# Performance work log

Hardware: AMD Instinct MI355X
Metric: run time of the kernel (lower is better)

The kernel has to match this reference:

```python
import jax, jax.numpy as jnp
import numpy as np

B, H, S, D = 4, 8, 2048, 64
NEG = -1e9


def setup_inputs() -> dict:
    key = jax.random.key(0)
    k1, k2, k3, k4 = jax.random.split(key, 4)
    qs = jax.random.normal(k1, (B, H, S, D), dtype=jnp.float32)
    ks = jax.random.normal(k2, (B, H, S, D), dtype=jnp.float32)
    vs = jax.random.normal(k3, (B, H, S, D), dtype=jnp.float32)
    # binary 0/1 float mask, broadcast over heads
    mask = (jax.random.uniform(k4, (B, 1, S, S)) < 0.5).astype(jnp.float32)
    return {"qs": qs, "ks": ks, "vs": vs, "mask": mask}


def reference(qs, ks, vs, mask):
    scale = 1.0 / np.sqrt(qs.shape[-1]).astype(np.float32)
    # [B,H,S,S] logits; multiplicative pre-mask, then additive -1e9 on masked slots
    logits = jnp.einsum('bhqd,bhkd->bhqk', qs, ks) * mask * scale
    logits = logits + (1.0 - mask) * NEG
    weights = jax.nn.softmax(logits, axis=-1) * mask  # multiplicative post-mask
    return jnp.einsum('bhqk,bhkd->bhqd', weights, vs)
```

## Files before the change

### kernel.cpp

```cpp
#include <hip/hip_runtime.h>
#include <stdint.h>

#define S_LEN 2048
#define NTILE 32

typedef float f32x4 __attribute__((ext_vector_type(4)));
typedef float f32x16 __attribute__((ext_vector_type(16)));
typedef short bf16x8 __attribute__((ext_vector_type(8)));

__device__ __forceinline__ uint16_t f2bf(float f) {
    uint32_t u = __float_as_uint(f);
    return (uint16_t)((u + 0x7FFFu + ((u >> 16) & 1u)) >> 16);
}

#define AS3PTR(p) ((__attribute__((address_space(3))) uint32_t*)(uintptr_t)(p))
#define AS1PTR(p) ((const __attribute__((address_space(1))) uint32_t*)(uintptr_t)(p))

__global__ __launch_bounds__(256)
void prep_all(const float* __restrict__ K, const float* __restrict__ V,
              const float* __restrict__ M, uint8_t* __restrict__ Kd,
              uint8_t* __restrict__ Vd, uint16_t* __restrict__ Mp)
{
    __shared__ float mt[4096];
    const int bid = blockIdx.x;
    const int tid = threadIdx.x;
    if (bid < 2048) {
        int flat = bid * 256 + tid;
        int s = flat & 511, tile = flat >> 9;
        int key = s >> 3, dc = (s >> 1) & 3, h = s & 1;
        int kt = tile & 31, bh = tile >> 5;
        const float* src = K + (((size_t)bh * S_LEN + kt * 64 + key) << 6) + dc * 16 + h * 8;
        f32x4 a = *(const f32x4*)src;
        f32x4 b = *(const f32x4*)(src + 4);
        bf16x8 o;
        o[0] = (short)f2bf(a[0]); o[1] = (short)f2bf(a[1]);
        o[2] = (short)f2bf(a[2]); o[3] = (short)f2bf(a[3]);
        o[4] = (short)f2bf(b[0]); o[5] = (short)f2bf(b[1]);
        o[6] = (short)f2bf(b[2]); o[7] = (short)f2bf(b[3]);
        *(bf16x8*)(Kd + ((size_t)tile << 13) + (((dc * 2 + h) * 64 + key) << 4)) = o;
    } else if (bid < 4096) {
        int flat = (bid - 2048) * 256 + tid;
        int s = flat & 511, tile = flat >> 9;
        int d = s & 63, h = (s >> 6) & 1, ku = s >> 7;
        int kt = tile & 31, bh = tile >> 5;
        const float* src = V + (((size_t)bh * S_LEN + kt * 64 + ku * 16 + h * 8) << 6) + d;
        bf16x8 o;
        #pragma unroll
        for (int j = 0; j < 8; ++j) o[j] = (short)f2bf(src[j << 6]);
        *(bf16x8*)(Vd + ((size_t)tile << 13) + (((ku * 2 + h) * 64 + d) << 4)) = o;
    } else {
        int mid = bid - 4096;
        int b = mid >> 10, qt = (mid >> 5) & 31, kt = mid & 31;
        int row = tid >> 2, cc = tid & 3;
        const float* src = M + ((size_t)(b * S_LEN + qt * 64 + row) * S_LEN) + kt * 64;
        #pragma unroll
        for (int i = 0; i < 4; ++i)
            *(f32x4*)&mt[(row << 6) + cc * 16 + i * 4] =
                *(const f32x4*)(src + cc * 16 + i * 4);
        __syncthreads();
        int l = tid & 63, w = tid >> 6;
        int qw = w >> 1, kw = w & 1, h = l >> 5, l31 = l & 31;
        uint32_t m = 0;
        #pragma unroll
        for (int r = 0; r < 16; ++r) {
            int keyl = 32 * kw + (r & 3) + 8 * (r >> 2) + 4 * h;
            m |= (mt[((32 * qw + l31) << 6) + keyl] > 0.5f) << r;
        }
        Mp[((size_t)mid << 8) + tid] = (uint16_t)m;
    }
}

__global__ __launch_bounds__(256, 3)
void attn_fwd(const float* __restrict__ Q, const uint8_t* __restrict__ Kd,
              const uint8_t* __restrict__ Vd, const uint16_t* __restrict__ Mp,
              float* __restrict__ O)
{
    __shared__ __align__(16) uint8_t lds[49152];

    const int tid  = threadIdx.x;
    const int lane = tid & 63;
    const int w    = tid >> 6;
    const int qw   = w >> 1;
    const int kw   = w & 1;
    const int h    = lane >> 5;
    const int l31  = lane & 31;

    const int bid0 = blockIdx.x;
    const int bid  = ((bid0 & 7) << 7) + (bid0 >> 3);
    const int bh  = bid >> 5;
    const int qt  = bid & 31;
    const int b   = bh >> 3;
    const int q0  = qt << 6;

    const float QSCL = 0.125f * 1.44269504088896340736f;
    bf16x8 qf[4];
    {
        const float* qrow = Q + (((size_t)bh * S_LEN + q0 + 32 * qw + l31) << 6);
        #pragma unroll
        for (int dc = 0; dc < 4; ++dc) {
            f32x4 a  = *(const f32x4*)(qrow + dc * 16 + h * 8);
            f32x4 b4 = *(const f32x4*)(qrow + dc * 16 + h * 8 + 4);
            bf16x8 f;
            f[0] = (short)f2bf(a[0] * QSCL);  f[1] = (short)f2bf(a[1] * QSCL);
            f[2] = (short)f2bf(a[2] * QSCL);  f[3] = (short)f2bf(a[3] * QSCL);
            f[4] = (short)f2bf(b4[0] * QSCL); f[5] = (short)f2bf(b4[1] * QSCL);
            f[6] = (short)f2bf(b4[2] * QSCL); f[7] = (short)f2bf(b4[3] * QSCL);
            qf[dc] = f;
        }
    }

    f32x16 acc[2];
    acc[0] = (f32x16)(0.f);
    acc[1] = (f32x16)(0.f);
    float lsum = 0.f;

    const uint8_t*  ksrc  = Kd + (((size_t)bh * 32) << 13) + (w << 10) + lane * 16;
    const uint8_t*  vsrc  = Vd + (((size_t)bh * 32) << 13) + (w << 10) + lane * 16;
    const uint16_t* mbase = Mp + (((size_t)(b * 32 + qt) * 32) << 8) + (w << 6) + lane;

    uint32_t mreg[3];

#define STAGE(T, SLOT)                                                          \
    {                                                                           \
        size_t toff = (size_t)(T) << 13;                                        \
        __builtin_amdgcn_global_load_lds(AS1PTR(ksrc + toff),                   \
            AS3PTR(&lds[(SLOT) * 16384 + (w << 10)]), 16, 0, 0);                \
        __builtin_amdgcn_global_load_lds(AS1PTR(ksrc + toff + 4096),            \
            AS3PTR(&lds[(SLOT) * 16384 + 4096 + (w << 10)]), 16, 0, 0);         \
        __builtin_amdgcn_global_load_lds(AS1PTR(vsrc + toff),                   \
            AS3PTR(&lds[(SLOT) * 16384 + 8192 + (w << 10)]), 16, 0, 0);         \
        __builtin_amdgcn_global_load_lds(AS1PTR(vsrc + toff + 4096),            \
            AS3PTR(&lds[(SLOT) * 16384 + 12288 + (w << 10)]), 16, 0, 0);        \
        mreg[SLOT] = mbase[(size_t)(T) << 8];                                   \
    }

#define COMPUTE(B)                                                              \
    {                                                                           \
        const uint8_t* kb   = &lds[(B) * 16384];                                \
        const uint8_t* vbuf = &lds[(B) * 16384 + 8192];                         \
        uint32_t mw = mreg[B];                                                  \
        f32x16 s = (f32x16)(0.f);                                               \
        __builtin_amdgcn_s_setprio(1);                                          \
        _Pragma("unroll")                                                       \
        for (int dc = 0; dc < 4; ++dc) {                                        \
            bf16x8 kf = *(const bf16x8*)(kb + (((dc * 2 + h) * 64 + 32 * kw + l31) << 4)); \
            s = __builtin_amdgcn_mfma_f32_32x32x16_bf16(kf, qf[dc], s, 0, 0, 0); \
        }                                                                       \
        __builtin_amdgcn_s_setprio(0);                                          \
        uint32_t pd[8];                                                         \
        _Pragma("unroll")                                                       \
        for (int rq = 0; rq < 8; ++rq) {                                        \
            float x0 = (mw & (1u << (2 * rq)))     ? s[2 * rq]     : -1000.f;   \
            float x1 = (mw & (1u << (2 * rq + 1))) ? s[2 * rq + 1] : -1000.f;   \
            float e0, e1;                                                       \
            asm("v_exp_f32 %0, %1" : "=v"(e0) : "v"(x0));                       \
            asm("v_exp_f32 %0, %1" : "=v"(e1) : "v"(x1));                       \
            lsum += e0 + e1;                                                    \
            asm("v_cvt_pk_bf16_f32 %0, %1, %2" : "=v"(pd[rq]) : "v"(e0), "v"(e1)); \
        }                                                                       \
        _Pragma("unroll")                                                       \
        for (int u = 0; u < 2; ++u) {                                           \
            asm("v_permlane32_swap_b32 %0, %1" : "+v"(pd[4*u]),   "+v"(pd[4*u+2])); \
            asm("v_permlane32_swap_b32 %0, %1" : "+v"(pd[4*u+1]), "+v"(pd[4*u+3])); \
        }                                                                       \
        __builtin_amdgcn_s_setprio(1);                                          \
        _Pragma("unroll")                                                       \
        for (int u = 0; u < 2; ++u) {                                           \
            union { uint32_t d[4]; bf16x8 v; } pa;                              \
            pa.d[0] = pd[4*u]; pa.d[1] = pd[4*u+1];                             \
            pa.d[2] = pd[4*u+2]; pa.d[3] = pd[4*u+3];                           \
            _Pragma("unroll")                                                   \
            for (int dblk = 0; dblk < 2; ++dblk) {                              \
                bf16x8 vf = *(const bf16x8*)(vbuf +                             \
                    ((((kw * 2 + u) * 2 + h) * 64 + 32 * dblk + l31) << 4));    \
                acc[dblk] = __builtin_amdgcn_mfma_f32_32x32x16_bf16(pa.v, vf, acc[dblk], 0, 0, 0); \
            }                                                                   \
        }                                                                       \
        __builtin_amdgcn_s_setprio(0);                                          \
    }

#define BODY(T, B, SLOT2, WN, DOSTAGE)                                          \
    {                                                                           \
        asm volatile("s_waitcnt vmcnt(" #WN ")" ::: "memory");                  \
        __builtin_amdgcn_s_barrier();                                           \
        __builtin_amdgcn_sched_barrier(0);                                      \
        if (DOSTAGE) STAGE((T) + 2, SLOT2);                                     \
        COMPUTE(B);                                                             \
    }

    STAGE(0, 0);
    STAGE(1, 1);

    #pragma unroll 1
    for (int it = 0; it < 10; ++it) {
        int t = it * 3;
        BODY(t,     0, 2, 5, true);
        BODY(t + 1, 1, 0, 5, true);
        BODY(t + 2, 2, 1, 5, true);
    }
    BODY(30, 0, 2, 5, false);
    BODY(31, 1, 2, 0, false);

#undef BODY
#undef COMPUTE
#undef STAGE

    lsum += __shfl_xor(lsum, 32, 64);

    __syncthreads();
    float* ex  = (float*)lds;
    float* ex2 = (float*)(lds + 16384);
    if (kw == 1) {
        #pragma unroll
        for (int dblk = 0; dblk < 2; ++dblk)
            #pragma unroll
            for (int rq = 0; rq < 4; ++rq) {
                f32x4 v = { acc[dblk][4 * rq], acc[dblk][4 * rq + 1],
                            acc[dblk][4 * rq + 2], acc[dblk][4 * rq + 3] };
                *(f32x4*)&ex[(qw << 11) + (((dblk << 2) + rq) << 8) + (lane << 2)] = v;
            }
        if (lane < 32) ex2[(qw << 5) + lane] = lsum;
    }
    __syncthreads();
    if (kw == 0) {
        #pragma unroll
        for (int dblk = 0; dblk < 2; ++dblk)
            #pragma unroll
            for (int rq = 0; rq < 4; ++rq) {
                f32x4 v = *(const f32x4*)&ex[(qw << 11) + (((dblk << 2) + rq) << 8) + (lane << 2)];
                acc[dblk][4 * rq]     += v[0];
                acc[dblk][4 * rq + 1] += v[1];
                acc[dblk][4 * rq + 2] += v[2];
                acc[dblk][4 * rq + 3] += v[3];
            }
        float l = lsum + ex2[(qw << 5) + l31];
        float linv = (l > 0.f) ? 1.f / l : 0.f;

        float* obase = O + (((size_t)bh * S_LEN + q0 + 32 * qw) << 6);
        #pragma unroll
        for (int r = 0; r < 16; ++r) {
            int qloc = (r & 3) + 8 * (r >> 2) + 4 * h;
            float inv = __shfl(linv, qloc, 64);
            obase[(qloc << 6) + l31]      = acc[0][r] * inv;
            obase[(qloc << 6) + 32 + l31] = acc[1][r] * inv;
        }
    }
}

extern "C" void kernel_launch(void* const* d_in, const int* in_sizes, int n_in,
                              void* d_out, int out_size, void* d_ws, size_t ws_size,
                              hipStream_t stream) {
    const float* qs   = (const float*)d_in[0];
    const float* ks   = (const float*)d_in[1];
    const float* vs   = (const float*)d_in[2];
    const float* mask = (const float*)d_in[3];
    float* out = (float*)d_out;
    (void)in_sizes; (void)n_in; (void)out_size; (void)ws_size;

    uint8_t* ws = (uint8_t*)d_ws;
    uint8_t* Kd = ws;
    uint8_t* Vd = ws + (8u << 20);
    uint16_t* Mp = (uint16_t*)(ws + (16u << 20));

    hipLaunchKernelGGL(prep_all, dim3(8192), dim3(256), 0, stream,
                       ks, vs, mask, Kd, Vd, Mp);
    hipLaunchKernelGGL(attn_fwd, dim3(1024), dim3(256), 0, stream,
                       qs, Kd, Vd, Mp, out);
}
```

Measured before the change: 80.36 us.

## Software-pipeline QK of next tile with softmax-PV of current, double-buffer LDS

Restructures the main loop so the QK^T MFMAs for tile t+1 are issued alongside the exp/PV work for tile t, with K and V staged separately into two double-buffered slots. This cuts LDS from 48KB to 32KB and raises the occupancy hint to four blocks per CU. Masking now applies a bitwise AND to exp outputs instead of selecting -1000 before the exponent. The exchange is a full vmcnt(0) wait every iteration and a second live score register set, which adds register pressure at the higher occupancy target.

```diff
diff --git a/kernel.cpp b/kernel.cpp
--- a/kernel.cpp
+++ b/kernel.cpp
@@ -70,12 +70,12 @@
     }
 }
 
-__global__ __launch_bounds__(256, 3)
+__global__ __launch_bounds__(256, 4)
 void attn_fwd(const float* __restrict__ Q, const uint8_t* __restrict__ Kd,
               const uint8_t* __restrict__ Vd, const uint16_t* __restrict__ Mp,
               float* __restrict__ O)
 {
-    __shared__ __align__(16) uint8_t lds[49152];
+    __shared__ __align__(16) uint8_t lds[32768];
 
     const int tid  = threadIdx.x;
     const int lane = tid & 63;
@@ -114,55 +114,66 @@
     acc[1] = (f32x16)(0.f);
     float lsum = 0.f;
 
-    const uint8_t*  ksrc  = Kd + (((size_t)bh * 32) << 13) + (w << 10) + lane * 16;
-    const uint8_t*  vsrc  = Vd + (((size_t)bh * 32) << 13) + (w << 10) + lane * 16;
-    const uint16_t* mbase = Mp + (((size_t)(b * 32 + qt) * 32) << 8) + (w << 6) + lane;
-
-    uint32_t mreg[3];
-
-#define STAGE(T, SLOT)                                                          \
+    const uint8_t*  kst = Kd + (((size_t)bh * 32) << 13) + (w << 10) + lane * 16;
+    const uint8_t*  vst = Vd + (((size_t)bh * 32) << 13) + (w << 10) + lane * 16;
+    const uint16_t* mst = Mp + (((size_t)(b * 32 + qt) * 32) << 8) + (w << 6) + lane;
+
+    uint32_t mreg[2];
+    f32x16 sA, sB;
+
+#define STAGE_K(T, SLOT)                                                        \
     {                                                                           \
         size_t toff = (size_t)(T) << 13;                                        \
-        __builtin_amdgcn_global_load_lds(AS1PTR(ksrc + toff),                   \
-            AS3PTR(&lds[(SLOT) * 16384 + (w << 10)]), 16, 0, 0);                \
-        __builtin_amdgcn_global_load_lds(AS1PTR(ksrc + toff + 4096),            \
-            AS3PTR(&lds[(SLOT) * 16384 + 4096 + (w << 10)]), 16, 0, 0);         \
-        __builtin_amdgcn_global_load_lds(AS1PTR(vsrc + toff),                   \
-            AS3PTR(&lds[(SLOT) * 16384 + 8192 + (w << 10)]), 16, 0, 0);         \
-        __builtin_amdgcn_global_load_lds(AS1PTR(vsrc + toff + 4096),            \
-            AS3PTR(&lds[(SLOT) * 16384 + 12288 + (w << 10)]), 16, 0, 0);        \
-        mreg[SLOT] = mbase[(size_t)(T) << 8];                                   \
-    }
-
-#define COMPUTE(B)                                                              \
-    {                                                                           \
-        const uint8_t* kb   = &lds[(B) * 16384];                                \
-        const uint8_t* vbuf = &lds[(B) * 16384 + 8192];                         \
-        uint32_t mw = mreg[B];                                                  \
-        f32x16 s = (f32x16)(0.f);                                               \
+        __builtin_amdgcn_global_load_lds(AS1PTR(kst + toff),                    \
+            AS3PTR(&lds[(SLOT) * 8192 + (w << 10)]), 16, 0, 0);                 \
+        __builtin_amdgcn_global_load_lds(AS1PTR(kst + toff + 4096),             \
+            AS3PTR(&lds[(SLOT) * 8192 + 4096 + (w << 10)]), 16, 0, 0);          \
+    }
+#define STAGE_V(T, SLOT)                                                        \
+    {                                                                           \
+        size_t toff = (size_t)(T) << 13;                                        \
+        __builtin_amdgcn_global_load_lds(AS1PTR(vst + toff),                    \
+            AS3PTR(&lds[16384 + (SLOT) * 8192 + (w << 10)]), 16, 0, 0);         \
+        __builtin_amdgcn_global_load_lds(AS1PTR(vst + toff + 4096),             \
+            AS3PTR(&lds[16384 + (SLOT) * 8192 + 4096 + (w << 10)]), 16, 0, 0);  \
+    }
+#define LOADM(T, R)  mreg[R] = mst[(size_t)(T) << 8];
+
+#define QK(SREG, PAR)                                                           \
+    {                                                                           \
+        const uint8_t* kb = &lds[(PAR) * 8192];                                 \
+        SREG = (f32x16)(0.f);                                                   \
         __builtin_amdgcn_s_setprio(1);                                          \
         _Pragma("unroll")                                                       \
         for (int dc = 0; dc < 4; ++dc) {                                        \
             bf16x8 kf = *(const bf16x8*)(kb + (((dc * 2 + h) * 64 + 32 * kw + l31) << 4)); \
-            s = __builtin_amdgcn_mfma_f32_32x32x16_bf16(kf, qf[dc], s, 0, 0, 0); \
+            SREG = __builtin_amdgcn_mfma_f32_32x32x16_bf16(kf, qf[dc], SREG, 0, 0, 0); \
         }                                                                       \
         __builtin_amdgcn_s_setprio(0);                                          \
+    }
+
+#define SMPV(SREG, PAR, MR)                                                     \
+    {                                                                           \
+        uint32_t mw = mreg[MR];                                                 \
         uint32_t pd[8];                                                         \
         _Pragma("unroll")                                                       \
         for (int rq = 0; rq < 8; ++rq) {                                        \
-            float x0 = (mw & (1u << (2 * rq)))     ? s[2 * rq]     : -1000.f;   \
-            float x1 = (mw & (1u << (2 * rq + 1))) ? s[2 * rq + 1] : -1000.f;   \
             float e0, e1;                                                       \
-            asm("v_exp_f32 %0, %1" : "=v"(e0) : "v"(x0));                       \
-            asm("v_exp_f32 %0, %1" : "=v"(e1) : "v"(x1));                       \
-            lsum += e0 + e1;                                                    \
-            asm("v_cvt_pk_bf16_f32 %0, %1, %2" : "=v"(pd[rq]) : "v"(e0), "v"(e1)); \
+            asm("v_exp_f32 %0, %1" : "=v"(e0) : "v"(SREG[2 * rq]));             \
+            asm("v_exp_f32 %0, %1" : "=v"(e1) : "v"(SREG[2 * rq + 1]));         \
+            int32_t m0 = ((int32_t)(mw << (31 - 2 * rq))) >> 31;                \
+            int32_t m1 = ((int32_t)(mw << (30 - 2 * rq))) >> 31;                \
+            float p0 = __int_as_float(__float_as_int(e0) & m0);                 \
+            float p1 = __int_as_float(__float_as_int(e1) & m1);                 \
+            lsum += p0; lsum += p1;                                             \
+            asm("v_cvt_pk_bf16_f32 %0, %1, %2" : "=v"(pd[rq]) : "v"(p0), "v"(p1)); \
         }                                                                       \
         _Pragma("unroll")                                                       \
         for (int u = 0; u < 2; ++u) {                                           \
             asm("v_permlane32_swap_b32 %0, %1" : "+v"(pd[4*u]),   "+v"(pd[4*u+2])); \
             asm("v_permlane32_swap_b32 %0, %1" : "+v"(pd[4*u+1]), "+v"(pd[4*u+3])); \
         }                                                                       \
+        const uint8_t* vbuf = &lds[16384 + (PAR) * 8192];                       \
         __builtin_amdgcn_s_setprio(1);                                          \
         _Pragma("unroll")                                                       \
         for (int u = 0; u < 2; ++u) {                                           \
@@ -179,31 +190,47 @@
         __builtin_amdgcn_s_setprio(0);                                          \
     }
 
-#define BODY(T, B, SLOT2, WN, DOSTAGE)                                          \
-    {                                                                           \
-        asm volatile("s_waitcnt vmcnt(" #WN ")" ::: "memory");                  \
-        __builtin_amdgcn_s_barrier();                                           \
-        __builtin_amdgcn_sched_barrier(0);                                      \
-        if (DOSTAGE) STAGE((T) + 2, SLOT2);                                     \
-        COMPUTE(B);                                                             \
-    }
-
-    STAGE(0, 0);
-    STAGE(1, 1);
+#define SYNC(N)                                                                 \
+    asm volatile("s_waitcnt vmcnt(" #N ")" ::: "memory");                       \
+    __builtin_amdgcn_s_barrier();                                               \
+    __builtin_amdgcn_sched_barrier(0);
+
+#define BODY(T, SP, SN, PAR, DOK)                                               \
+    {                                                                           \
+        SYNC(0);                                                                \
+        STAGE_V((T) + 1, (PAR) ^ 1);                                            \
+        if (DOK) STAGE_K((T) + 2, PAR);                                         \
+        LOADM((T) + 1, (PAR) ^ 1);                                              \
+        QK(SN, (PAR) ^ 1);                                                      \
+        SMPV(SP, PAR, PAR);                                                     \
+    }
+
+    STAGE_K(0, 0);
+    STAGE_V(0, 0);
+    STAGE_K(1, 1);
+    LOADM(0, 0);
+    asm volatile("s_waitcnt vmcnt(5)" ::: "memory");
+    __builtin_amdgcn_s_barrier();
+    __builtin_amdgcn_sched_barrier(0);
+    QK(sA, 0);
 
     #pragma unroll 1
-    for (int it = 0; it < 10; ++it) {
-        int t = it * 3;
-        BODY(t,     0, 2, 5, true);
-        BODY(t + 1, 1, 0, 5, true);
-        BODY(t + 2, 2, 1, 5, true);
-    }
-    BODY(30, 0, 2, 5, false);
-    BODY(31, 1, 2, 0, false);
+    for (int i = 0; i < 15; ++i) {
+        int t = i * 2;
+        BODY(t,     sA, sB, 0, true);
+        BODY(t + 1, sB, sA, 1, true);
+    }
+    BODY(30, sA, sB, 0, false);
+    SYNC(0);
+    SMPV(sB, 1, 1);
 
 #undef BODY
-#undef COMPUTE
-#undef STAGE
+#undef SYNC
+#undef SMPV
+#undef QK
+#undef LOADM
+#undef STAGE_V
+#undef STAGE_K
 
     lsum += __shfl_xor(lsum, 32, 64);
 
```

Result: no change. 80.82 us (+0.6%).
